# Kernel tuning notes

Measured on AMD Instinct MI355X. Metric: run time of the kernel, lower is better.

## Reference

```python
import jax, jax.numpy as jnp
import numpy as np

Z_DIM = 1          # coord column zeroed before coalescing (module default)
GRID = 512         # max coordinate value per column (exclusive)


def setup_inputs() -> dict:
    key = jax.random.key(0)
    k1, k2 = jax.random.split(key)
    N, C = 400000, 128
    features = jax.random.normal(k1, (N, C), dtype=jnp.float32)
    coords = jax.random.randint(k2, (N, 4), 0, GRID, dtype=jnp.int32)
    return {"features": features, "coords": coords}


def reference(features, coords):
    # features: [N, C] float, coords: [N, 4] int32
    N = features.shape[0]
    # Zero the z column (BEV flattening), as in flatten_coords[:, z_dim] = 0.
    # Since the z column is identically 0 after zeroing, coalescing the 4-col
    # coords is equivalent to keying on the remaining 3 columns.
    non_z = [i for i in range(4) if i != Z_DIM]
    c0 = coords[:, non_z[0]].astype(jnp.int32)
    c1 = coords[:, non_z[1]].astype(jnp.int32)
    c2 = coords[:, non_z[2]].astype(jnp.int32)
    lin_key = (c0 * GRID + c1) * GRID + c2  # < 512^3 < 2^31, fits int32

    # coalesce(): unique coords + scatter-add of [count | features]
    uniq, inv = jnp.unique(lin_key, size=N, fill_value=-1, return_inverse=True)
    ones = jnp.ones((N, 1), dtype=features.dtype)
    feat_with_cnt = jnp.concatenate([ones, features], axis=1)  # [N, C+1]
    sums = jax.ops.segment_sum(feat_with_cnt, inv.reshape(-1), num_segments=N)  # [N, C+1]

    cnt = sums[:, :1]
    out_features = sums[:, 1:] / jnp.maximum(cnt, 1.0)  # padded rows have cnt=0 -> stay 0

    # Decode unique keys back to 4-column coords (z column = 0).
    d2 = uniq % GRID
    rem = uniq // GRID
    d1 = rem % GRID
    d0 = rem // GRID
    zeros = jnp.zeros_like(d0)
    cols = [None] * 4
    cols[Z_DIM] = zeros
    cols[non_z[0]] = d0
    cols[non_z[1]] = d1
    cols[non_z[2]] = d2
    out_coords = jnp.stack(cols, axis=1).astype(jnp.int32)  # [N, 4], padded rows negative

    return out_features, out_coords, cnt[:, 0]
```

## Files before the change

kernel.cpp:

```cpp
#include <hip/hip_runtime.h>


#define NWORDS      (1u << 22)
#define SCAN_BLOCKS 1024
#define WPB         (NWORDS / SCAN_BLOCKS)
#define WPT         (WPB / 256)

typedef float f32x4 __attribute__((ext_vector_type(4)));
typedef unsigned u32;

__global__ void k_build(const int4* __restrict__ coords, u32* __restrict__ bitmap,
                        u32* __restrict__ keys, float* __restrict__ cnt,
                        u32* __restrict__ ctrs, int N) {
    int i = blockIdx.x * blockDim.x + threadIdx.x;
    if (i == 0) { ctrs[0] = 0u; ctrs[1] = 0u; }
    if (i >= N) return;
    int4 c = coords[i];
    u32 key = ((u32)c.x << 18) | ((u32)c.z << 9) | (u32)c.w;
    keys[i] = key;
    cnt[i] = 0.0f;
    atomicOr(&bitmap[key >> 5], 1u << (key & 31u));
}

__global__ void k_scan1(const u32* __restrict__ bitmap, u32* __restrict__ blockSums) {
    __shared__ u32 sd[256];
    const uint4* bm = (const uint4*)(bitmap + (size_t)blockIdx.x * WPB + (size_t)threadIdx.x * WPT);
    u32 s = 0;
#pragma unroll
    for (int k = 0; k < WPT / 4; ++k) {
        uint4 v = bm[k];
        s += __popc(v.x) + __popc(v.y) + __popc(v.z) + __popc(v.w);
    }
    sd[threadIdx.x] = s;
    __syncthreads();
    for (int off = 128; off > 0; off >>= 1) {
        if ((int)threadIdx.x < off) sd[threadIdx.x] += sd[threadIdx.x + off];
        __syncthreads();
    }
    if (threadIdx.x == 0) blockSums[blockIdx.x] = sd[0];
}

__global__ void k_scan2(const u32* __restrict__ blockSums,
                        u32* __restrict__ blockOffsets,
                        u32* __restrict__ totalM) {
    __shared__ u32 sd[SCAN_BLOCKS];
    int t = threadIdx.x;
    u32 v = blockSums[t];
    sd[t] = v;
    __syncthreads();
    for (int off = 1; off < SCAN_BLOCKS; off <<= 1) {
        u32 add = (t >= off) ? sd[t - off] : 0u;
        __syncthreads();
        sd[t] += add;
        __syncthreads();
    }
    blockOffsets[t] = sd[t] - v;
    if (t == SCAN_BLOCKS - 1) totalM[0] = sd[t];
}

__global__ void k_scan3enum(const u32* __restrict__ bitmap,
                            const u32* __restrict__ blockOffsets,
                            uint2* __restrict__ pairs,
                            float4* __restrict__ outc) {
    __shared__ u32 sd[256];
    size_t base = (size_t)blockIdx.x * WPB + (size_t)threadIdx.x * WPT;
    const uint4* bm = (const uint4*)(bitmap + base);
    u32 w[WPT];
    u32 s = 0;
#pragma unroll
    for (int k = 0; k < WPT / 4; ++k) {
        uint4 v = bm[k];
        w[k * 4 + 0] = v.x; w[k * 4 + 1] = v.y; w[k * 4 + 2] = v.z; w[k * 4 + 3] = v.w;
        s += __popc(v.x) + __popc(v.y) + __popc(v.z) + __popc(v.w);
    }
    int t = threadIdx.x;
    sd[t] = s;
    __syncthreads();
    for (int off = 1; off < 256; off <<= 1) {
        u32 add = (t >= off) ? sd[t - off] : 0u;
        __syncthreads();
        sd[t] += add;
        __syncthreads();
    }
    u32 run = blockOffsets[blockIdx.x] + sd[t] - s;
#pragma unroll
    for (int k = 0; k < WPT; ++k) {
        u32 bits = w[k];
        pairs[base + k] = make_uint2(run, bits);
        while (bits) {
            int b = __ffs(bits) - 1;
            u32 key = ((u32)(base + k) << 5) | (u32)b;
            outc[run] = make_float4((float)(key >> 18), 0.f,
                                    (float)((key >> 9) & 511u), (float)(key & 511u));
            ++run;
            bits &= bits - 1u;
        }
    }
}

__global__ void __launch_bounds__(256) k_scatter(
        const f32x4* __restrict__ fin, const u32* __restrict__ keys,
        const uint2* __restrict__ pairs, float* __restrict__ cnt,
        u32* __restrict__ srcElem, uint2* __restrict__ dupElem,
        u32* __restrict__ dupSeg, u32* __restrict__ ctrs,
        f32x4* __restrict__ fout, int N) {
    int gid = blockIdx.x * blockDim.x + threadIdx.x;
    int elem = gid >> 5;
    if (elem >= N) return;
    int c4 = gid & 31;
    u32 s = 0;
    if ((threadIdx.x & 31) == 0) {
        u32 key = keys[elem];
        uint2 p = pairs[key >> 5];
        s = p.x + __popc(p.y & ((1u << (key & 31u)) - 1u));
        float old = atomicAdd(&cnt[s], 1.0f);
        if (old == 0.0f) {
            srcElem[s] = (u32)elem;
        } else {
            u32 di = atomicAdd(&ctrs[0], 1u);
            dupElem[di] = make_uint2((u32)elem, s);
            if (old == 1.0f) {
                u32 ds = atomicAdd(&ctrs[1], 1u);
                dupSeg[ds] = s;
            }
        }
    }
    s = (u32)__shfl((int)s, threadIdx.x & 32);
    f32x4 v = __builtin_nontemporal_load(&fin[(size_t)elem * 32 + c4]);
    __builtin_nontemporal_store(v, &fout[(size_t)s * 32 + c4]);
}

__global__ void k_fix1(const u32* __restrict__ dupSeg, const u32* __restrict__ ctrs,
                       const u32* __restrict__ totalM,
                       f32x4* __restrict__ fout, float4* __restrict__ outc, int N) {
    u32 nds = ctrs[1];
    u32 M = totalM[0];
    u32 npad = (u32)N - M;
    u32 total = nds + npad;
    int gid = blockIdx.x * blockDim.x + threadIdx.x;
    int c4 = gid & 31;
    u32 stride = (gridDim.x * blockDim.x) >> 5;
    f32x4 z = {0.f, 0.f, 0.f, 0.f};
    for (u32 r = (u32)(gid >> 5); r < total; r += stride) {
        u32 row;
        bool pad = (r >= nds);
        row = pad ? (M + r - nds) : dupSeg[r];
        fout[(size_t)row * 32 + c4] = z;
        if (pad && c4 == 0) outc[row] = make_float4(-1.f, 0.f, 511.f, 511.f);
    }
}

__global__ void k_fix2(const f32x4* __restrict__ fin, const uint2* __restrict__ dupElem,
                       const u32* __restrict__ dupSeg, const u32* __restrict__ srcElem,
                       const float* __restrict__ cnt, const u32* __restrict__ ctrs,
                       f32x4* __restrict__ fout) {
    u32 nde = ctrs[0], nds = ctrs[1];
    u32 total = nde + nds;
    int gid = blockIdx.x * blockDim.x + threadIdx.x;
    int c4 = gid & 31;
    u32 stride = (gridDim.x * blockDim.x) >> 5;
    for (u32 t = (u32)(gid >> 5); t < total; t += stride) {
        u32 e, s;
        if (t < nde) { uint2 d = dupElem[t]; e = d.x; s = d.y; }
        else         { s = dupSeg[t - nde]; e = srcElem[s]; }
        float inv = 1.0f / cnt[s];
        f32x4 v = fin[(size_t)e * 32 + c4];
        float* dst = (float*)&fout[(size_t)s * 32 + c4];
        atomicAdd(dst + 0, v.x * inv);
        atomicAdd(dst + 1, v.y * inv);
        atomicAdd(dst + 2, v.z * inv);
        atomicAdd(dst + 3, v.w * inv);
    }
}

extern "C" void kernel_launch(void* const* d_in, const int* in_sizes, int n_in,
                              void* d_out, int out_size, void* d_ws, size_t ws_size,
                              hipStream_t stream) {
    const f32x4* feat_in = (const f32x4*)d_in[0];
    const int4* coords = (const int4*)d_in[1];
    int N = in_sizes[1] / 4;

    float* out = (float*)d_out;
    f32x4* out_feat = (f32x4*)out;
    float4* out_coords = (float4*)(out + (size_t)N * 128);
    float* out_cnt = out + (size_t)N * 132;

    u32* keys = (u32*)d_ws;
    u32* srcElem = keys + N;
    u32* blockSums = srcElem + N;
    u32* blockOffsets = blockSums + SCAN_BLOCKS;
    u32* totalM = blockOffsets + SCAN_BLOCKS;
    u32* ctrs = totalM + 1;
    u32* dupSeg = ctrs + 8;
    uint2* dupElem = (uint2*)(dupSeg + 65536);
    u32* bitmap = (u32*)(dupElem + 65536);
    uint2* pairs = (uint2*)(bitmap + NWORDS);

    int nb = (N + 255) / 256;

    hipMemsetAsync(bitmap, 0, (size_t)NWORDS * 4, stream);

    k_build<<<nb, 256, 0, stream>>>(coords, bitmap, keys, out_cnt, ctrs, N);
    k_scan1<<<SCAN_BLOCKS, 256, 0, stream>>>(bitmap, blockSums);
    k_scan2<<<1, SCAN_BLOCKS, 0, stream>>>(blockSums, blockOffsets, totalM);
    k_scan3enum<<<SCAN_BLOCKS, 256, 0, stream>>>(bitmap, blockOffsets, pairs, out_coords);
    k_scatter<<<(int)(((size_t)N * 32 + 255) / 256), 256, 0, stream>>>(
        feat_in, keys, pairs, out_cnt, srcElem, dupElem, dupSeg, ctrs, out_feat, N);
    k_fix1<<<256, 256, 0, stream>>>(dupSeg, ctrs, totalM, out_feat, out_coords, N);
    k_fix2<<<256, 256, 0, stream>>>(feat_in, dupElem, dupSeg, srcElem, out_cnt, ctrs, out_feat);
}
```

Measured before the change: 169.9 us.

## Split segment lookup into its own kernel and mark duplicate segments with a bitmask

Segment-id computation and counting move out of the wide scatter kernel into a new per-element kernel that writes a seg array, records duplicated segments in a dupBits bitmask and appends them to dupSeg. The scatter then only reads seg, with no lane-0 atomics or shuffle. The duplicate-fix kernel now scans all N elements, checks the bitmask and accumulates whole rows with one thread per element, replacing the dupElem/srcElem lists. This adds a launch and an N-wide pass over seg, and one thread doing 128 serial atomics per duplicate row may be slower than the old 32-lane-per-row layout.

After: 187.3 us. 1.1x slower.

```diff
diff --git a/kernel.cpp b/kernel.cpp
--- a/kernel.cpp
+++ b/kernel.cpp
@@ -11,9 +11,10 @@
 
 __global__ void k_build(const int4* __restrict__ coords, u32* __restrict__ bitmap,
                         u32* __restrict__ keys, float* __restrict__ cnt,
-                        u32* __restrict__ ctrs, int N) {
+                        u32* __restrict__ dupBits, u32* __restrict__ ctrs, int N) {
     int i = blockIdx.x * blockDim.x + threadIdx.x;
-    if (i == 0) { ctrs[0] = 0u; ctrs[1] = 0u; }
+    if (i < 16384) dupBits[i] = 0u;
+    if (i == 0) ctrs[1] = 0u;
     if (i >= N) return;
     int4 c = coords[i];
     u32 key = ((u32)c.x << 18) | ((u32)c.z << 9) | (u32)c.w;
@@ -98,34 +99,32 @@
     }
 }
 
+__global__ void k_seg(const u32* __restrict__ keys, const uint2* __restrict__ pairs,
+                      float* __restrict__ cnt, u32* __restrict__ seg,
+                      u32* __restrict__ dupSeg, u32* __restrict__ dupBits,
+                      u32* __restrict__ ctrs, int N) {
+    int i = blockIdx.x * blockDim.x + threadIdx.x;
+    if (i >= N) return;
+    u32 key = keys[i];
+    uint2 p = pairs[key >> 5];
+    u32 s = p.x + __popc(p.y & ((1u << (key & 31u)) - 1u));
+    seg[i] = s;
+    float old = atomicAdd(&cnt[s], 1.0f);
+    if (old == 1.0f) {
+        u32 ds = atomicAdd(&ctrs[1], 1u);
+        dupSeg[ds] = s;
+        atomicOr(&dupBits[s >> 5], 1u << (s & 31u));
+    }
+}
+
 __global__ void __launch_bounds__(256) k_scatter(
-        const f32x4* __restrict__ fin, const u32* __restrict__ keys,
-        const uint2* __restrict__ pairs, float* __restrict__ cnt,
-        u32* __restrict__ srcElem, uint2* __restrict__ dupElem,
-        u32* __restrict__ dupSeg, u32* __restrict__ ctrs,
+        const f32x4* __restrict__ fin, const u32* __restrict__ seg,
         f32x4* __restrict__ fout, int N) {
     int gid = blockIdx.x * blockDim.x + threadIdx.x;
     int elem = gid >> 5;
     if (elem >= N) return;
     int c4 = gid & 31;
-    u32 s = 0;
-    if ((threadIdx.x & 31) == 0) {
-        u32 key = keys[elem];
-        uint2 p = pairs[key >> 5];
-        s = p.x + __popc(p.y & ((1u << (key & 31u)) - 1u));
-        float old = atomicAdd(&cnt[s], 1.0f);
-        if (old == 0.0f) {
-            srcElem[s] = (u32)elem;
-        } else {
-            u32 di = atomicAdd(&ctrs[0], 1u);
-            dupElem[di] = make_uint2((u32)elem, s);
-            if (old == 1.0f) {
-                u32 ds = atomicAdd(&ctrs[1], 1u);
-                dupSeg[ds] = s;
-            }
-        }
-    }
-    s = (u32)__shfl((int)s, threadIdx.x & 32);
+    u32 s = seg[elem];
     f32x4 v = __builtin_nontemporal_load(&fin[(size_t)elem * 32 + c4]);
     __builtin_nontemporal_store(v, &fout[(size_t)s * 32 + c4]);
 }
@@ -142,34 +141,30 @@
     u32 stride = (gridDim.x * blockDim.x) >> 5;
     f32x4 z = {0.f, 0.f, 0.f, 0.f};
     for (u32 r = (u32)(gid >> 5); r < total; r += stride) {
-        u32 row;
         bool pad = (r >= nds);
-        row = pad ? (M + r - nds) : dupSeg[r];
+        u32 row = pad ? (M + r - nds) : dupSeg[r];
         fout[(size_t)row * 32 + c4] = z;
         if (pad && c4 == 0) outc[row] = make_float4(-1.f, 0.f, 511.f, 511.f);
     }
 }
 
-__global__ void k_fix2(const f32x4* __restrict__ fin, const uint2* __restrict__ dupElem,
-                       const u32* __restrict__ dupSeg, const u32* __restrict__ srcElem,
-                       const float* __restrict__ cnt, const u32* __restrict__ ctrs,
-                       f32x4* __restrict__ fout) {
-    u32 nde = ctrs[0], nds = ctrs[1];
-    u32 total = nde + nds;
-    int gid = blockIdx.x * blockDim.x + threadIdx.x;
-    int c4 = gid & 31;
-    u32 stride = (gridDim.x * blockDim.x) >> 5;
-    for (u32 t = (u32)(gid >> 5); t < total; t += stride) {
-        u32 e, s;
-        if (t < nde) { uint2 d = dupElem[t]; e = d.x; s = d.y; }
-        else         { s = dupSeg[t - nde]; e = srcElem[s]; }
-        float inv = 1.0f / cnt[s];
-        f32x4 v = fin[(size_t)e * 32 + c4];
-        float* dst = (float*)&fout[(size_t)s * 32 + c4];
-        atomicAdd(dst + 0, v.x * inv);
-        atomicAdd(dst + 1, v.y * inv);
-        atomicAdd(dst + 2, v.z * inv);
-        atomicAdd(dst + 3, v.w * inv);
+__global__ void k_fix2(const f32x4* __restrict__ fin, const u32* __restrict__ seg,
+                       const float* __restrict__ cnt, const u32* __restrict__ dupBits,
+                       f32x4* __restrict__ fout, int N) {
+    int i = blockIdx.x * blockDim.x + threadIdx.x;
+    if (i >= N) return;
+    u32 s = seg[i];
+    if (!(dupBits[s >> 5] & (1u << (s & 31u)))) return;
+    float inv = 1.0f / cnt[s];
+    const f32x4* src = &fin[(size_t)i * 32];
+    float* dst = (float*)&fout[(size_t)s * 32];
+#pragma unroll 4
+    for (int c = 0; c < 32; ++c) {
+        f32x4 v = src[c];
+        atomicAdd(dst + c * 4 + 0, v.x * inv);
+        atomicAdd(dst + c * 4 + 1, v.y * inv);
+        atomicAdd(dst + c * 4 + 2, v.z * inv);
+        atomicAdd(dst + c * 4 + 3, v.w * inv);
     }
 }
 
@@ -185,27 +180,28 @@
     float4* out_coords = (float4*)(out + (size_t)N * 128);
     float* out_cnt = out + (size_t)N * 132;
 
-    u32* keys = (u32*)d_ws;
-    u32* srcElem = keys + N;
-    u32* blockSums = srcElem + N;
+    u32* bitmap = (u32*)d_ws;
+    uint2* pairs = (uint2*)(bitmap + NWORDS);
+    u32* keys = (u32*)(pairs + NWORDS);
+    u32* seg = keys + N;
+    u32* dupSeg = seg + N;
+    u32* dupBits = dupSeg + 65536;
+    u32* blockSums = dupBits + 16384;
     u32* blockOffsets = blockSums + SCAN_BLOCKS;
     u32* totalM = blockOffsets + SCAN_BLOCKS;
     u32* ctrs = totalM + 1;
-    u32* dupSeg = ctrs + 8;
-    uint2* dupElem = (uint2*)(dupSeg + 65536);
-    u32* bitmap = (u32*)(dupElem + 65536);
-    uint2* pairs = (uint2*)(bitmap + NWORDS);
 
     int nb = (N + 255) / 256;
 
     hipMemsetAsync(bitmap, 0, (size_t)NWORDS * 4, stream);
 
-    k_build<<<nb, 256, 0, stream>>>(coords, bitmap, keys, out_cnt, ctrs, N);
+    k_build<<<nb, 256, 0, stream>>>(coords, bitmap, keys, out_cnt, dupBits, ctrs, N);
     k_scan1<<<SCAN_BLOCKS, 256, 0, stream>>>(bitmap, blockSums);
     k_scan2<<<1, SCAN_BLOCKS, 0, stream>>>(blockSums, blockOffsets, totalM);
     k_scan3enum<<<SCAN_BLOCKS, 256, 0, stream>>>(bitmap, blockOffsets, pairs, out_coords);
+    k_seg<<<nb, 256, 0, stream>>>(keys, pairs, out_cnt, seg, dupSeg, dupBits, ctrs, N);
     k_scatter<<<(int)(((size_t)N * 32 + 255) / 256), 256, 0, stream>>>(
-        feat_in, keys, pairs, out_cnt, srcElem, dupElem, dupSeg, ctrs, out_feat, N);
+        feat_in, seg, out_feat, N);
     k_fix1<<<256, 256, 0, stream>>>(dupSeg, ctrs, totalM, out_feat, out_coords, N);
-    k_fix2<<<256, 256, 0, stream>>>(feat_in, dupElem, dupSeg, srcElem, out_cnt, ctrs, out_feat);
-}
+    k_fix2<<<nb, 256, 0, stream>>>(feat_in, seg, out_cnt, dupBits, out_feat, N);
+}
```

## Fuse bitmap scan kernels with last-block global scan and compact rank index

Applied to the files above, without the earlier changes.

Merges the three scan kernels into one. Each block computes its popcount prefix, the last-arriving block scans the per-block sums, and the others spin on a flag before enumerating coordinates. The per-word (offset, bits) pairs array is replaced by one offset per 8 words, and scatter recomputes the rank from the bitmap with popcounts. This removes a second bitmap pass, two launches and a large pairs write, but relies on all blocks being co-resident for the spin-wait and adds lookup work in scatter.

New measurement: 218.4 us. 28.5% more time.

```diff
diff --git a/kernel.cpp b/kernel.cpp
--- a/kernel.cpp
+++ b/kernel.cpp
@@ -5,6 +5,7 @@
 #define SCAN_BLOCKS 1024
 #define WPB         (NWORDS / SCAN_BLOCKS)
 #define WPT         (WPB / 256)
+#define NGROUPS     (NWORDS / 8)
 
 typedef float f32x4 __attribute__((ext_vector_type(4)));
 typedef unsigned u32;
@@ -13,7 +14,7 @@
                         u32* __restrict__ keys, float* __restrict__ cnt,
                         u32* __restrict__ ctrs, int N) {
     int i = blockIdx.x * blockDim.x + threadIdx.x;
-    if (i == 0) { ctrs[0] = 0u; ctrs[1] = 0u; }
+    if (i < 4) ctrs[i] = 0u;
     if (i >= N) return;
     int4 c = coords[i];
     u32 key = ((u32)c.x << 18) | ((u32)c.z << 9) | (u32)c.w;
@@ -22,49 +23,18 @@
     atomicOr(&bitmap[key >> 5], 1u << (key & 31u));
 }
 
-__global__ void k_scan1(const u32* __restrict__ bitmap, u32* __restrict__ blockSums) {
+__global__ void __launch_bounds__(256, 4) k_scan(
+        const u32* __restrict__ bitmap, u32* __restrict__ off8,
+        float4* __restrict__ outc, u32* __restrict__ blockSums,
+        u32* __restrict__ blockOffsets, u32* __restrict__ totalM,
+        u32* __restrict__ ctrs) {
     __shared__ u32 sd[256];
-    const uint4* bm = (const uint4*)(bitmap + (size_t)blockIdx.x * WPB + (size_t)threadIdx.x * WPT);
-    u32 s = 0;
-#pragma unroll
-    for (int k = 0; k < WPT / 4; ++k) {
-        uint4 v = bm[k];
-        s += __popc(v.x) + __popc(v.y) + __popc(v.z) + __popc(v.w);
-    }
-    sd[threadIdx.x] = s;
-    __syncthreads();
-    for (int off = 128; off > 0; off >>= 1) {
-        if ((int)threadIdx.x < off) sd[threadIdx.x] += sd[threadIdx.x + off];
-        __syncthreads();
-    }
-    if (threadIdx.x == 0) blockSums[blockIdx.x] = sd[0];
-}
-
-__global__ void k_scan2(const u32* __restrict__ blockSums,
-                        u32* __restrict__ blockOffsets,
-                        u32* __restrict__ totalM) {
-    __shared__ u32 sd[SCAN_BLOCKS];
-    int t = threadIdx.x;
-    u32 v = blockSums[t];
-    sd[t] = v;
-    __syncthreads();
-    for (int off = 1; off < SCAN_BLOCKS; off <<= 1) {
-        u32 add = (t >= off) ? sd[t - off] : 0u;
-        __syncthreads();
-        sd[t] += add;
-        __syncthreads();
-    }
-    blockOffsets[t] = sd[t] - v;
-    if (t == SCAN_BLOCKS - 1) totalM[0] = sd[t];
-}
-
-__global__ void k_scan3enum(const u32* __restrict__ bitmap,
-                            const u32* __restrict__ blockOffsets,
-                            uint2* __restrict__ pairs,
-                            float4* __restrict__ outc) {
-    __shared__ u32 sd[256];
-    size_t base = (size_t)blockIdx.x * WPB + (size_t)threadIdx.x * WPT;
+    __shared__ u32 sFlag;
+    const int t = threadIdx.x;
+    const int bid = blockIdx.x;
+    const size_t base = (size_t)bid * WPB + (size_t)t * WPT;
     const uint4* bm = (const uint4*)(bitmap + base);
+
     u32 w[WPT];
     u32 s = 0;
 #pragma unroll
@@ -73,7 +43,6 @@
         w[k * 4 + 0] = v.x; w[k * 4 + 1] = v.y; w[k * 4 + 2] = v.z; w[k * 4 + 3] = v.w;
         s += __popc(v.x) + __popc(v.y) + __popc(v.z) + __popc(v.w);
     }
-    int t = threadIdx.x;
     sd[t] = s;
     __syncthreads();
     for (int off = 1; off < 256; off <<= 1) {
@@ -82,28 +51,80 @@
         sd[t] += add;
         __syncthreads();
     }
-    u32 run = blockOffsets[blockIdx.x] + sd[t] - s;
-#pragma unroll
-    for (int k = 0; k < WPT; ++k) {
-        u32 bits = w[k];
-        pairs[base + k] = make_uint2(run, bits);
-        while (bits) {
-            int b = __ffs(bits) - 1;
-            u32 key = ((u32)(base + k) << 5) | (u32)b;
-            outc[run] = make_float4((float)(key >> 18), 0.f,
-                                    (float)((key >> 9) & 511u), (float)(key & 511u));
-            ++run;
-            bits &= bits - 1u;
+    const u32 myExcl = sd[t] - s;
+    const u32 blockTotal = sd[255];
+
+    if (t == 0) {
+        __hip_atomic_store(&blockSums[bid], blockTotal, __ATOMIC_RELAXED,
+                           __HIP_MEMORY_SCOPE_AGENT);
+        u32 ticket = __hip_atomic_fetch_add(&ctrs[2], 1u, __ATOMIC_ACQ_REL,
+                                            __HIP_MEMORY_SCOPE_AGENT);
+        sFlag = (ticket == SCAN_BLOCKS - 1) ? 1u : 0u;
+    }
+    __syncthreads();
+
+    if (sFlag) {
+        u32 v0 = __hip_atomic_load(&blockSums[t * 4 + 0], __ATOMIC_RELAXED, __HIP_MEMORY_SCOPE_AGENT);
+        u32 v1 = __hip_atomic_load(&blockSums[t * 4 + 1], __ATOMIC_RELAXED, __HIP_MEMORY_SCOPE_AGENT);
+        u32 v2 = __hip_atomic_load(&blockSums[t * 4 + 2], __ATOMIC_RELAXED, __HIP_MEMORY_SCOPE_AGENT);
+        u32 v3 = __hip_atomic_load(&blockSums[t * 4 + 3], __ATOMIC_RELAXED, __HIP_MEMORY_SCOPE_AGENT);
+        u32 ls = v0 + v1 + v2 + v3;
+        __syncthreads();
+        sd[t] = ls;
+        __syncthreads();
+        for (int off = 1; off < 256; off <<= 1) {
+            u32 add = (t >= off) ? sd[t - off] : 0u;
+            __syncthreads();
+            sd[t] += add;
+            __syncthreads();
+        }
+        u32 ex = sd[t] - ls;
+        __hip_atomic_store(&blockOffsets[t * 4 + 0], ex,            __ATOMIC_RELAXED, __HIP_MEMORY_SCOPE_AGENT);
+        __hip_atomic_store(&blockOffsets[t * 4 + 1], ex + v0,       __ATOMIC_RELAXED, __HIP_MEMORY_SCOPE_AGENT);
+        __hip_atomic_store(&blockOffsets[t * 4 + 2], ex + v0 + v1,  __ATOMIC_RELAXED, __HIP_MEMORY_SCOPE_AGENT);
+        __hip_atomic_store(&blockOffsets[t * 4 + 3], ex + v0 + v1 + v2, __ATOMIC_RELAXED, __HIP_MEMORY_SCOPE_AGENT);
+        if (t == 255) totalM[0] = sd[255];
+        __syncthreads();
+        if (t == 0)
+            __hip_atomic_store(&ctrs[3], 1u, __ATOMIC_RELEASE, __HIP_MEMORY_SCOPE_AGENT);
+    } else {
+        if (t == 0) {
+            while (__hip_atomic_load(&ctrs[3], __ATOMIC_ACQUIRE,
+                                     __HIP_MEMORY_SCOPE_AGENT) == 0u) {
+                __builtin_amdgcn_s_sleep(2);
+            }
+        }
+        __syncthreads();
+    }
+
+    u32 run = __hip_atomic_load(&blockOffsets[bid], __ATOMIC_RELAXED,
+                                __HIP_MEMORY_SCOPE_AGENT) + myExcl;
+
+    u32 g0 = (u32)bid * (WPB / 8) + (u32)t * 2;
+#pragma unroll
+    for (int h = 0; h < 2; ++h) {
+        off8[g0 + h] = run;
+#pragma unroll
+        for (int k = h * 8; k < h * 8 + 8; ++k) {
+            u32 bits = w[k];
+            while (bits) {
+                int b = __ffs(bits) - 1;
+                u32 key = ((u32)(base + k) << 5) | (u32)b;
+                outc[run] = make_float4((float)(key >> 18), 0.f,
+                                        (float)((key >> 9) & 511u), (float)(key & 511u));
+                ++run;
+                bits &= bits - 1u;
+            }
         }
     }
 }
 
 __global__ void __launch_bounds__(256) k_scatter(
         const f32x4* __restrict__ fin, const u32* __restrict__ keys,
-        const uint2* __restrict__ pairs, float* __restrict__ cnt,
-        u32* __restrict__ srcElem, uint2* __restrict__ dupElem,
-        u32* __restrict__ dupSeg, u32* __restrict__ ctrs,
-        f32x4* __restrict__ fout, int N) {
+        const u32* __restrict__ off8, const uint4* __restrict__ bm4,
+        float* __restrict__ cnt, u32* __restrict__ srcElem,
+        uint2* __restrict__ dupElem, u32* __restrict__ dupSeg,
+        u32* __restrict__ ctrs, f32x4* __restrict__ fout, int N) {
     int gid = blockIdx.x * blockDim.x + threadIdx.x;
     int elem = gid >> 5;
     if (elem >= N) return;
@@ -111,8 +132,18 @@
     u32 s = 0;
     if ((threadIdx.x & 31) == 0) {
         u32 key = keys[elem];
-        uint2 p = pairs[key >> 5];
-        s = p.x + __popc(p.y & ((1u << (key & 31u)) - 1u));
+        u32 g = key >> 8;
+        u32 widx = (key >> 5) & 7u;
+        u32 mask = (1u << (key & 31u)) - 1u;
+        uint4 a = bm4[g * 2], b = bm4[g * 2 + 1];
+        u32 wv[8] = {a.x, a.y, a.z, a.w, b.x, b.y, b.z, b.w};
+        u32 r = off8[g];
+#pragma unroll
+        for (u32 k = 0; k < 8; ++k) {
+            u32 m = (k < widx) ? 0xFFFFFFFFu : ((k == widx) ? mask : 0u);
+            r += __popc(wv[k] & m);
+        }
+        s = r;
         float old = atomicAdd(&cnt[s], 1.0f);
         if (old == 0.0f) {
             srcElem[s] = (u32)elem;
@@ -142,9 +173,8 @@
     u32 stride = (gridDim.x * blockDim.x) >> 5;
     f32x4 z = {0.f, 0.f, 0.f, 0.f};
     for (u32 r = (u32)(gid >> 5); r < total; r += stride) {
-        u32 row;
         bool pad = (r >= nds);
-        row = pad ? (M + r - nds) : dupSeg[r];
+        u32 row = pad ? (M + r - nds) : dupSeg[r];
         fout[(size_t)row * 32 + c4] = z;
         if (pad && c4 == 0) outc[row] = make_float4(-1.f, 0.f, 511.f, 511.f);
     }
@@ -185,27 +215,27 @@
     float4* out_coords = (float4*)(out + (size_t)N * 128);
     float* out_cnt = out + (size_t)N * 132;
 
-    u32* keys = (u32*)d_ws;
+    u32* bitmap = (u32*)d_ws;
+    u32* off8 = bitmap + NWORDS;
+    u32* keys = off8 + NGROUPS;
     u32* srcElem = keys + N;
-    u32* blockSums = srcElem + N;
+    u32* dupSeg = srcElem + N;
+    uint2* dupElem = (uint2*)(dupSeg + 131072);
+    u32* blockSums = (u32*)(dupElem + 131072);
     u32* blockOffsets = blockSums + SCAN_BLOCKS;
     u32* totalM = blockOffsets + SCAN_BLOCKS;
     u32* ctrs = totalM + 1;
-    u32* dupSeg = ctrs + 8;
-    uint2* dupElem = (uint2*)(dupSeg + 65536);
-    u32* bitmap = (u32*)(dupElem + 65536);
-    uint2* pairs = (uint2*)(bitmap + NWORDS);
 
     int nb = (N + 255) / 256;
 
     hipMemsetAsync(bitmap, 0, (size_t)NWORDS * 4, stream);
 
     k_build<<<nb, 256, 0, stream>>>(coords, bitmap, keys, out_cnt, ctrs, N);
-    k_scan1<<<SCAN_BLOCKS, 256, 0, stream>>>(bitmap, blockSums);
-    k_scan2<<<1, SCAN_BLOCKS, 0, stream>>>(blockSums, blockOffsets, totalM);
-    k_scan3enum<<<SCAN_BLOCKS, 256, 0, stream>>>(bitmap, blockOffsets, pairs, out_coords);
+    k_scan<<<SCAN_BLOCKS, 256, 0, stream>>>(bitmap, off8, out_coords, blockSums,
+                                            blockOffsets, totalM, ctrs);
     k_scatter<<<(int)(((size_t)N * 32 + 255) / 256), 256, 0, stream>>>(
-        feat_in, keys, pairs, out_cnt, srcElem, dupElem, dupSeg, ctrs, out_feat, N);
+        feat_in, keys, off8, (const uint4*)bitmap, out_cnt, srcElem,
+        dupElem, dupSeg, ctrs, out_feat, N);
     k_fix1<<<256, 256, 0, stream>>>(dupSeg, ctrs, totalM, out_feat, out_coords, N);
     k_fix2<<<256, 256, 0, stream>>>(feat_in, dupElem, dupSeg, srcElem, out_cnt, ctrs, out_feat);
 }
```
